# Optimization experiments

Hardware: AMD Instinct MI355X
Metric: run time of the kernel (lower is better)

The kernel has to match this reference:

```python
import jax, jax.numpy as jnp
import numpy as np

B, S, D_MODEL = 2, 2048, 768
N_QK, D_QK = 16, 16
N_OV, D_OV = 256, 1
VKV = 16
ROT_DIM, ROT_BASE = 16, 10000.0
SCALE = D_QK ** 0.5  # attn_scale defaults to sqrt(d_qk_head)


def _rotary_sin_cos(n_ctx, rotary_dim, base):
    # TransformerLens-style, non-adjacent pairs (GPT-NeoX)
    pos = jnp.arange(n_ctx, dtype=jnp.float32)
    dim = jnp.arange(rotary_dim // 2, dtype=jnp.float32)
    freq = base ** (dim / (rotary_dim / 2))
    freq = jnp.concatenate([freq, freq])  # 'd -> (2 d)'
    angles = pos[:, None] / freq[None, :]  # [n_ctx, rotary_dim]
    return jnp.sin(angles), jnp.cos(angles)


def _apply_rotary(x, sin, cos):
    # x: [B, S, H, d_head]; rotate first ROT_DIM dims, pass through the rest
    s = x.shape[1]
    xr = x[..., :ROT_DIM]
    half = ROT_DIM // 2
    rot = jnp.concatenate([-xr[..., half:], xr[..., :half]], axis=-1)  # rotate_every_two (non-adjacent)
    xr = xr * cos[:s, None, :] + rot * sin[:s, None, :]
    return jnp.concatenate([xr, x[..., ROT_DIM:]], axis=-1) if x.shape[-1] > ROT_DIM else xr


def setup_inputs() -> dict:
    key = jax.random.key(0)
    ks = jax.random.split(key, 6)
    std_qk = np.sqrt(2.0 / (D_MODEL * D_QK))   # kaiming fan_in for [H, d_model, d_head]
    std_v = np.sqrt(2.0 / (D_MODEL * D_OV))
    std_o = np.sqrt(2.0 / (D_OV * D_MODEL))
    std_vk = np.sqrt(2.0 / (N_QK * D_QK))
    return {
        "resid": jax.random.normal(ks[0], (B, S, D_MODEL), jnp.float32),
        "W_Q": jax.random.normal(ks[1], (N_QK, D_MODEL, D_QK), jnp.float32) * std_qk,
        "W_K": jax.random.normal(ks[2], (N_QK, D_MODEL, D_QK), jnp.float32) * std_qk,
        "W_V": jax.random.normal(ks[3], (N_OV, D_MODEL, D_OV), jnp.float32) * std_v,
        "W_O": jax.random.normal(ks[4], (N_OV, D_OV, D_MODEL), jnp.float32) * std_o,
        "b_Q": jnp.zeros((N_QK, D_QK), jnp.float32),
        "b_K": jnp.zeros((N_QK, D_QK), jnp.float32),
        "b_V": jnp.zeros((N_OV, D_OV), jnp.float32),
        "b_O": jnp.zeros((D_MODEL,), jnp.float32),
        "virtual_k": jax.random.normal(ks[5], (VKV, N_QK, D_QK), jnp.float32) * std_vk,
        "virtual_v": jnp.zeros((VKV, N_OV, D_OV), jnp.float32),
    }


def reference(resid, W_Q, W_K, W_V, W_O, b_Q, b_K, b_V, b_O, virtual_k, virtual_v):
    b, s, _ = resid.shape
    sin, cos = _rotary_sin_cos(s, ROT_DIM, ROT_BASE)

    q = jnp.einsum('bsd,hde->bshe', resid, W_Q) + b_Q  # [B,S,N_QK,D_QK]
    k = jnp.einsum('bsd,hde->bshe', resid, W_K) + b_K
    v = jnp.einsum('bsd,hde->bshe', resid, W_V) + b_V  # [B,S,N_OV,1]

    q = _apply_rotary(q, sin, cos)
    k = _apply_rotary(k, sin, cos)

    # append virtual KV along key axis
    k = jnp.concatenate([k, jnp.broadcast_to(virtual_k[None], (b, VKV, N_QK, D_QK))], axis=1)
    v = jnp.concatenate([v, jnp.broadcast_to(virtual_v[None], (b, VKV, N_OV, D_OV))], axis=1)

    scores = jnp.einsum('bqhe,bkhe->bhqk', q, k) / SCALE  # [B,H,S,S+VKV]
    i = jnp.arange(s)[:, None]
    j = jnp.arange(s + VKV)[None, :]
    mask = (j - i) <= VKV  # tril(.., diagonal=VKV)
    scores = jnp.where(mask, scores, -jnp.inf)
    pattern = jax.nn.softmax(scores, axis=-1)
    pattern = jnp.where(jnp.isnan(pattern), 0.0, pattern)

    r = N_OV // N_QK
    v_r = v.transpose(0, 2, 1, 3).reshape(b, N_QK, r, s + VKV, D_OV)  # [B,n_qk,r,K,1]
    z = jnp.einsum('bnqk,bnrkh->bnrqh', pattern, v_r)  # [B,n_qk,r,S,1]
    z = z.reshape(b, N_OV, s, D_OV).transpose(0, 2, 1, 3)  # [B,S,N_OV,1]

    out = jnp.einsum('bqhd,hdm->bqm', z, W_O) + b_O  # [B,S,D_MODEL]
    return out
```

## Files before the change

kernel.cpp:

```cpp
#include <hip/hip_runtime.h>
#include <hip/hip_bf16.h>
#include <math.h>

#define B_   2
#define S_   2048
#define DM   768
#define H_   16
#define C_   256
#define VKV_ 16
#define SK   2064
#define SKP  2080
#define NT_  65

#define TSPLIT 16
#define MAXSP  5
#define NACT   164

typedef __attribute__((ext_vector_type(8))) short short8;
typedef __attribute__((ext_vector_type(4))) short short4v;
typedef __attribute__((ext_vector_type(4))) float f32x4;
typedef __attribute__((ext_vector_type(16))) float f32x16;
typedef __attribute__((ext_vector_type(4))) unsigned uint4v;

#define QSCALE 0.360673760222240851f
#define L2B8   1.6609640474436811f

__device__ __forceinline__ short tobf(float f) {
    union { float f; unsigned u; } x; x.f = f;
    unsigned r = x.u + 0x7FFFu + ((x.u >> 16) & 1u);
    return (short)(r >> 16);
}
__device__ __forceinline__ float frombf_lo(unsigned u) {
    union { unsigned u; float f; } x; x.u = u << 16; return x.f;
}
__device__ __forceinline__ float frombf_hi(unsigned u) {
    union { unsigned u; float f; } x; x.u = u & 0xFFFF0000u; return x.f;
}

__device__ __forceinline__ void gload_lds16(const short* g, short* l) {
    __builtin_amdgcn_global_load_lds(
        (const __attribute__((address_space(1))) unsigned int*)g,
        (__attribute__((address_space(3))) unsigned int*)l, 16, 0, 0);
}

#define NRES (4096*768/4)
#define NWQ  (768*768)
#define NWO  (768*256)
__global__ __launch_bounds__(256) void conv_all(
    const float* __restrict__ resid,
    const float* __restrict__ WQ, const float* __restrict__ WK,
    const float* __restrict__ WV, const float* __restrict__ WO,
    const float* __restrict__ bQ, const float* __restrict__ bK,
    const float* __restrict__ bV,
    const float* __restrict__ vKp, const float* __restrict__ vVp,
    short* __restrict__ Ab, short* __restrict__ Wqkv_t,
    short* __restrict__ WtO, float* __restrict__ bqkv,
    short* __restrict__ Kb2, short* __restrict__ Vt3)
{
    int t = blockIdx.x * 256 + threadIdx.x;
    if (t < NRES) {
        float4 v = *(const float4*)(resid + (size_t)t * 4);
        short4v o = { tobf(v.x), tobf(v.y), tobf(v.z), tobf(v.w) };
        *(short4v*)(Ab + (size_t)t * 4) = o;
        return;
    }
    t -= NRES;
    if (t < NWQ) {
        int cc, d;
        if (t < 512 * 768) {
            const int e    = t & 15;
            const int rest = t >> 4;
            d  = rest % 768;
            cc = (rest / 768) * 16 + e;
        } else { cc = t / 768; d = t % 768; }
        float w;
        if (cc < 256)      w = WQ[((size_t)(cc >> 4) * DM + d) * 16 + (cc & 15)];
        else if (cc < 512) w = WK[((size_t)((cc - 256) >> 4) * DM + d) * 16 + (cc & 15)];
        else               w = WV[(size_t)(cc - 512) * DM + d];
        Wqkv_t[(size_t)cc * 768 + d] = tobf(w);
        return;
    }
    t -= NWQ;
    if (t < NWO) {
        int c = t & 255, m = t >> 8;
        WtO[t] = tobf(WO[(size_t)c * DM + m]);
        return;
    }
    t -= NWO;
    if (t < 768) {
        bqkv[t] = (t < 256) ? bQ[t] : (t < 512 ? bK[t - 256] : bV[t - 512]);
        return;
    }
    t -= 768;
    if (t < 32 * 32) {
        const int bh = t >> 5;
        const int s  = S_ + (t & 31);
        const int h  = bh & 15;
        short kb[16], vb[16];
        if (s < SK) {
            const int tt = s - S_;
#pragma unroll
            for (int e = 0; e < 16; ++e) {
                kb[e] = tobf(vKp[(size_t)tt * 256 + h * 16 + e]);
                vb[e] = tobf(vVp[(size_t)tt * 256 + h * 16 + e]);
            }
        } else {
#pragma unroll
            for (int e = 0; e < 16; ++e) { kb[e] = 0; vb[e] = 0; }
        }
        const int t5 = s >> 5;
        short* kbase = Kb2 + ((size_t)bh * NT_ + t5) * 512 + (s & 31) * 8;
#pragma unroll
        for (int e = 0; e < 8; ++e)  { kbase[e] = kb[e]; kbase[256 + e] = kb[e + 8]; }
        short* vbase = Vt3 + ((size_t)bh * NT_ + t5) * 1024
                     + ((s >> 4) & 1) * 512 + ((s >> 3) & 1) * 8 + (s & 7);
#pragma unroll
        for (int dv = 0; dv < 16; ++dv) vbase[dv * 16] = vb[dv];
    }
}

__global__ __launch_bounds__(256) void mm_qkv(
    const short* __restrict__ A, const short* __restrict__ Bt,
    const float* __restrict__ bias,
    short* __restrict__ Qb2, short* __restrict__ Kb2, short* __restrict__ Vt3)
{
    __shared__ float CtS[128][65];
    short* As = (short*)&CtS[0][0];
    short* Bs = (short*)&CtS[0][0] + 8192;

    const int tid  = threadIdx.x;
    const int w    = tid >> 6;
    const int lane = tid & 63;
    const int wm   = w >> 1, wn = w & 1;
    const int g    = lane >> 4, c = lane & 15;

    const int linear = blockIdx.y * 12 + blockIdx.x;
    const int xcd  = linear & 7;
    const int jj2  = linear >> 3;
    const int m0   = (xcd * 4 + jj2 / 12) * 128;
    const int n0   = (jj2 % 12) * 64;

    f32x4 acc[4][2];
#pragma unroll
    for (int i = 0; i < 4; ++i)
#pragma unroll
        for (int j = 0; j < 2; ++j) acc[i][j] = (f32x4){0.f, 0.f, 0.f, 0.f};

    const int lr = lane >> 3;
    const int lc = lane & 7;

    for (int k0 = 0; k0 < 768; k0 += 64) {
#pragma unroll
        for (int i = 0; i < 4; ++i) {
            const int ch  = i * 4 + w;
            const int row = ch * 8 + lr;
            const int scc = lc ^ (row & 7);
            gload_lds16(A + (size_t)(m0 + row) * 768 + k0 + scc * 8, As + ch * 512);
        }
#pragma unroll
        for (int i = 0; i < 2; ++i) {
            const int ch  = i * 4 + w;
            const int row = ch * 8 + lr;
            const int scc = lc ^ (row & 7);
            gload_lds16(Bt + (size_t)(n0 + row) * 768 + k0 + scc * 8, Bs + ch * 512);
        }
        __syncthreads();
#pragma unroll
        for (int kk = 0; kk < 64; kk += 32) {
            short8 af[4], bf[2];
#pragma unroll
            for (int i = 0; i < 4; ++i) {
                const int row = wm * 64 + i * 16 + c;
                const int sc  = ((kk >> 3) + g) ^ (row & 7);
                af[i] = *(const short8*)(As + row * 64 + sc * 8);
            }
#pragma unroll
            for (int j = 0; j < 2; ++j) {
                const int row = wn * 32 + j * 16 + c;
                const int sc  = ((kk >> 3) + g) ^ (row & 7);
                bf[j] = *(const short8*)(Bs + row * 64 + sc * 8);
            }
#pragma unroll
            for (int i = 0; i < 4; ++i)
#pragma unroll
                for (int j = 0; j < 2; ++j)
                    acc[i][j] = __builtin_amdgcn_mfma_f32_16x16x32_bf16(
                        af[i], bf[j], acc[i][j], 0, 0, 0);
        }
        __syncthreads();
    }

#pragma unroll
    for (int i = 0; i < 4; ++i)
#pragma unroll
        for (int j = 0; j < 2; ++j)
#pragma unroll
            for (int r = 0; r < 4; ++r)
                CtS[wm * 64 + i * 16 + 4 * g + r][wn * 32 + j * 16 + c] = acc[i][j][r];
    __syncthreads();

    const int b = m0 >> 11;
    if (n0 < 512) {
        const int isQ   = n0 < 256;
        const int hbase = (n0 & 255) >> 4;
#pragma unroll
        for (int it = 0; it < 2; ++it) {
            const int idx  = it * 256 + tid;
            const int srow = idx & 127;
            const int g16  = idx >> 7;
            const int s    = (m0 + srow) & 2047;
            const int bh   = b * 16 + hbase + g16;
            float v[16];
#pragma unroll
            for (int e = 0; e < 16; ++e)
                v[e] = CtS[srow][g16 * 16 + e] + bias[n0 + g16 * 16 + e];
            union { short s[16]; short8 v8[2]; } u;
#pragma unroll
            for (int e = 0; e < 8; ++e) {
                const float invf = __builtin_amdgcn_exp2f(-(float)e * L2B8);
                float sn, cs;
                __sincosf((float)s * invf, &sn, &cs);
                float o0 = v[e] * cs - v[e + 8] * sn;
                float o1 = v[e + 8] * cs + v[e] * sn;
                if (isQ) { o0 *= QSCALE; o1 *= QSCALE; }
                u.s[e] = tobf(o0); u.s[e + 8] = tobf(o1);
            }
            short* dst = (isQ ? Qb2 + ((size_t)bh * 64 + (s >> 5)) * 512
                              : Kb2 + ((size_t)bh * NT_ + (s >> 5)) * 512)
                       + (s & 31) * 8;
            *(short8*)dst         = u.v8[0];
            *(short8*)(dst + 256) = u.v8[1];
        }
    } else {
        const int hbase = (n0 - 512) >> 4;
#pragma unroll
        for (int it = 0; it < 2; ++it) {
            const int idx = it * 256 + tid;
            const int dvl = idx & 63;
            const int rg  = idx >> 6;
            const int s0  = (m0 + rg * 16) & 2047;
            const int bh  = b * 16 + hbase + (dvl >> 4);
            const float bv = bias[n0 + dvl];
            union { short s[16]; short8 v8[2]; } u;
#pragma unroll
            for (int k = 0; k < 16; ++k)
                u.s[k] = tobf(CtS[rg * 16 + k][dvl] + bv);
            short* dst = Vt3 + ((size_t)bh * NT_ + (s0 >> 5)) * 1024
                       + ((s0 >> 4) & 1) * 512 + (dvl & 15) * 16;
            *(short8*)dst       = u.v8[0];
            *(short8*)(dst + 8) = u.v8[1];
        }
    }
}

__global__ __launch_bounds__(256) void mm_out(
    const short* __restrict__ A, const short* __restrict__ Bt,
    const float* __restrict__ bias, float* __restrict__ Cout)
{
    __shared__ short As[128 * 64];
    __shared__ short Bs[64 * 64];

    const int tid  = threadIdx.x;
    const int w    = tid >> 6;
    const int lane = tid & 63;
    const int wm   = w >> 1, wn = w & 1;
    const int g    = lane >> 4, c = lane & 15;

    const int linear = blockIdx.y * 12 + blockIdx.x;
    const int xcd  = linear & 7;
    const int jj2  = linear >> 3;
    const int m0   = (xcd * 4 + jj2 / 12) * 128;
    const int n0   = (jj2 % 12) * 64;

    f32x4 acc[4][2];
#pragma unroll
    for (int i = 0; i < 4; ++i)
#pragma unroll
        for (int j = 0; j < 2; ++j) acc[i][j] = (f32x4){0.f, 0.f, 0.f, 0.f};

    const int lr = lane >> 3;
    const int lc = lane & 7;

    for (int k0 = 0; k0 < 256; k0 += 64) {
#pragma unroll
        for (int i = 0; i < 4; ++i) {
            const int ch  = i * 4 + w;
            const int row = ch * 8 + lr;
            const int scc = lc ^ (row & 7);
            gload_lds16(A + (size_t)(m0 + row) * 256 + k0 + scc * 8, As + ch * 512);
        }
#pragma unroll
        for (int i = 0; i < 2; ++i) {
            const int ch  = i * 4 + w;
            const int row = ch * 8 + lr;
            const int scc = lc ^ (row & 7);
            gload_lds16(Bt + (size_t)(n0 + row) * 256 + k0 + scc * 8, Bs + ch * 512);
        }
        __syncthreads();
#pragma unroll
        for (int kk = 0; kk < 64; kk += 32) {
            short8 af[4], bf[2];
#pragma unroll
            for (int i = 0; i < 4; ++i) {
                const int row = wm * 64 + i * 16 + c;
                const int sc  = ((kk >> 3) + g) ^ (row & 7);
                af[i] = *(const short8*)(As + row * 64 + sc * 8);
            }
#pragma unroll
            for (int j = 0; j < 2; ++j) {
                const int row = wn * 32 + j * 16 + c;
                const int sc  = ((kk >> 3) + g) ^ (row & 7);
                bf[j] = *(const short8*)(Bs + row * 64 + sc * 8);
            }
#pragma unroll
            for (int i = 0; i < 4; ++i)
#pragma unroll
                for (int j = 0; j < 2; ++j)
                    acc[i][j] = __builtin_amdgcn_mfma_f32_16x16x32_bf16(
                        af[i], bf[j], acc[i][j], 0, 0, 0);
        }
        __syncthreads();
    }
#pragma unroll
    for (int i = 0; i < 4; ++i)
#pragma unroll
        for (int j = 0; j < 2; ++j) {
            const int col = n0 + wn * 32 + j * 16 + c;
            const float bv = bias[col];
#pragma unroll
            for (int r = 0; r < 4; ++r) {
                const int row = m0 + wm * 64 + i * 16 + 4 * g + r;
                Cout[(size_t)row * DM + col] = acc[i][j][r] + bv;
            }
        }
}

__global__ __launch_bounds__(256) void attn_split(
    const short* __restrict__ Qb2, const short* __restrict__ Kb2,
    const short* __restrict__ Vt3, unsigned* __restrict__ PartA,
    float* __restrict__ PartL)
{
    const int w    = threadIdx.x >> 6;
    const int lane = threadIdx.x & 63;
    const int blk  = blockIdx.x;
    const int xcd  = blk & 7;
    const int j    = blk >> 3;
    const int bhl  = j / 41;
    const int slot = j - bhl * 41;
    const int bh   = xcd * 4 + bhl;
    const int r    = slot * 4 + w;
    int qt, sp;
    if (r < 49)       { sp = 1; qt = 15 + r; }
    else if (r < 82)  { sp = 2; qt = 31 + (r - 49); }
    else if (r < 99)  { sp = 3; qt = 47 + (r - 82); }
    else if (r == 99) { sp = 4; qt = 63; }
    else              { sp = 0; qt = 163 - r; }

    const int nt   = qt + 2;
    const int t0   = sp * TSPLIT;
    const int tend = min(t0 + TSPLIT, nt);

    const int hi = lane >> 5;
    const int qc = lane & 31;
    const int q0 = qt * 32;

    const f32x16 zero16 = {0,0,0,0,0,0,0,0,0,0,0,0,0,0,0,0};

    short8 qf = *(const short8*)(Qb2 + ((size_t)bh * 64 + qt) * 512 + lane * 8);

    f32x16 acc = zero16;
    float lsum = 0.f;

    const short* kbase = Kb2 + (size_t)bh * NT_ * 512 + lane * 8;
    const short* vbase = Vt3 + (size_t)bh * NT_ * 1024 + (lane & 15) * 16 + hi * 8;
    const int qv16  = q0 + qc + 16;
    const int tmask = (q0 + 17) >> 5;

#define LK(tt)  (*(const short8*)(kbase + (size_t)(tt) * 512))
#define LVA(tt) (*(const short8*)(vbase + (size_t)(tt) * 1024))
#define LVB(tt) (*(const short8*)(vbase + (size_t)(tt) * 1024 + 512))

#define SOFTMAX_TILE(S, tt, B1, B2)                                          \
    {                                                                        \
        if ((tt) >= tmask) {                                                 \
            const int kt_ = (tt) * 32;                                       \
            _Pragma("unroll")                                                \
            for (int rr = 0; rr < 16; ++rr) {                                \
                const int key = kt_ + (rr & 3) + 8 * (rr >> 2) + 4 * hi;     \
                S[rr] = (key <= qv16) ? S[rr] : -INFINITY;                   \
            }                                                                \
        }                                                                    \
        unsigned pk[8];                                                      \
        _Pragma("unroll")                                                    \
        for (int jj = 0; jj < 8; ++jj) {                                     \
            const float p0 = __builtin_amdgcn_exp2f(S[2 * jj]);              \
            const float p1 = __builtin_amdgcn_exp2f(S[2 * jj + 1]);          \
            lsum += p0 + p1;                                                 \
            asm("v_cvt_pk_bf16_f32 %0, %1, %2" : "=v"(pk[jj]) : "v"(p0), "v"(p1)); \
        }                                                                    \
        unsigned a0 = pk[0], a2 = pk[2], a1 = pk[1], a3 = pk[3];             \
        unsigned a4 = pk[4], a6 = pk[6], a5 = pk[5], a7 = pk[7];             \
        asm("v_permlane32_swap_b32 %0, %1" : "+v"(a0), "+v"(a2));            \
        asm("v_permlane32_swap_b32 %0, %1" : "+v"(a1), "+v"(a3));            \
        asm("v_permlane32_swap_b32 %0, %1" : "+v"(a4), "+v"(a6));            \
        asm("v_permlane32_swap_b32 %0, %1" : "+v"(a5), "+v"(a7));            \
        B1.u[0] = a0; B1.u[1] = a1; B1.u[2] = a2; B1.u[3] = a3;              \
        B2.u[0] = a4; B2.u[1] = a5; B2.u[2] = a6; B2.u[3] = a7;              \
    }

    const int npair_end = t0 + ((tend - t0) & ~1);

    if (t0 < npair_end) {
        short8 kfA = LK(t0),     vaA = LVA(t0),     vvA = LVB(t0);
        short8 kfB = LK(t0 + 1), vaB = LVA(t0 + 1), vvB = LVB(t0 + 1);

        for (int t = t0; t < npair_end; t += 2) {
            short8 kfA_n = kfA, vaA_n = vaA, vvA_n = vvA;
            short8 kfB_n = kfB, vaB_n = vaB, vvB_n = vvB;
            if (t + 2 < npair_end) {
                kfA_n = LK(t + 2); vaA_n = LVA(t + 2); vvA_n = LVB(t + 2);
                kfB_n = LK(t + 3); vaB_n = LVA(t + 3); vvB_n = LVB(t + 3);
            }

            __builtin_amdgcn_s_setprio(1);
            f32x16 S0 = __builtin_amdgcn_mfma_f32_32x32x16_bf16(kfA, qf, zero16, 0, 0, 0);
            f32x16 S1 = __builtin_amdgcn_mfma_f32_32x32x16_bf16(kfB, qf, zero16, 0, 0, 0);
            __builtin_amdgcn_s_setprio(0);

            union { unsigned u[4]; short8 v; } b1A, b2A, b1B, b2B;
            SOFTMAX_TILE(S0, t,     b1A, b2A);
            SOFTMAX_TILE(S1, t + 1, b1B, b2B);

            __builtin_amdgcn_s_setprio(1);
            acc = __builtin_amdgcn_mfma_f32_32x32x16_bf16(vaA, b1A.v, acc, 0, 0, 0);
            acc = __builtin_amdgcn_mfma_f32_32x32x16_bf16(vvA, b2A.v, acc, 0, 0, 0);
            acc = __builtin_amdgcn_mfma_f32_32x32x16_bf16(vaB, b1B.v, acc, 0, 0, 0);
            acc = __builtin_amdgcn_mfma_f32_32x32x16_bf16(vvB, b2B.v, acc, 0, 0, 0);
            __builtin_amdgcn_s_setprio(0);

            kfA = kfA_n; vaA = vaA_n; vvA = vvA_n;
            kfB = kfB_n; vaB = vaB_n; vvB = vvB_n;
        }
    }
    if (npair_end < tend) {
        const int t = npair_end;
        short8 kf = LK(t), va = LVA(t), vv = LVB(t);
        f32x16 S0 = __builtin_amdgcn_mfma_f32_32x32x16_bf16(kf, qf, zero16, 0, 0, 0);
        union { unsigned u[4]; short8 v; } b1, b2;
        SOFTMAX_TILE(S0, t, b1, b2);
        acc = __builtin_amdgcn_mfma_f32_32x32x16_bf16(va, b1.v, acc, 0, 0, 0);
        acc = __builtin_amdgcn_mfma_f32_32x32x16_bf16(vv, b2.v, acc, 0, 0, 0);
    }

    uint4v pa;
    asm("v_cvt_pk_bf16_f32 %0, %1, %2" : "=v"(pa.x) : "v"(acc[0]), "v"(acc[1]));
    asm("v_cvt_pk_bf16_f32 %0, %1, %2" : "=v"(pa.y) : "v"(acc[2]), "v"(acc[3]));
    asm("v_cvt_pk_bf16_f32 %0, %1, %2" : "=v"(pa.z) : "v"(acc[4]), "v"(acc[5]));
    asm("v_cvt_pk_bf16_f32 %0, %1, %2" : "=v"(pa.w) : "v"(acc[6]), "v"(acc[7]));

    const int pidx = (bh * 64 + qt) * MAXSP + sp;
    *(uint4v*)(PartA + ((size_t)pidx * 64 + lane) * 4) = pa;

    lsum += __shfl_xor(lsum, 32);
    if (hi == 0) PartL[(size_t)pidx * 32 + qc] = lsum;
}

__global__ __launch_bounds__(256) void attn_combine(
    const unsigned* __restrict__ PartA, const float* __restrict__ PartL,
    short* __restrict__ Zb)
{
    const int w    = threadIdx.x >> 6;
    const int lane = threadIdx.x & 63;
    const int wid  = blockIdx.x * 4 + w;
    const int bh   = wid >> 6;
    const int qt   = wid & 63;
    const int hi   = lane >> 5;
    const int qc   = lane & 31;
    const int ns   = (qt + 2 + TSPLIT - 1) / TSPLIT;

    float a[8];
#pragma unroll
    for (int rr = 0; rr < 8; ++rr) a[rr] = 0.f;
    float lsum = 0.f;

    const int pbase = (bh * 64 + qt) * MAXSP;
    for (int sp = 0; sp < ns; ++sp) {
        uint4v pa = *(const uint4v*)(PartA + ((size_t)(pbase + sp) * 64 + lane) * 4);
        a[0] += frombf_lo(pa.x); a[1] += frombf_hi(pa.x);
        a[2] += frombf_lo(pa.y); a[3] += frombf_hi(pa.y);
        a[4] += frombf_lo(pa.z); a[5] += frombf_hi(pa.z);
        a[6] += frombf_lo(pa.w); a[7] += frombf_hi(pa.w);
        lsum += PartL[(size_t)(pbase + sp) * 32 + qc];
    }
    const float inv = 1.f / lsum;

    const int b = bh >> 4, h = bh & 15;
    const int q0 = qt * 32;
    short* zp = Zb + ((size_t)(b * S_ + q0 + qc)) * C_ + h * 16;
    unsigned o01, o23, o45, o67;
    {
        float a0 = a[0] * inv, a1 = a[1] * inv, a2 = a[2] * inv, a3 = a[3] * inv;
        float a4 = a[4] * inv, a5 = a[5] * inv, a6 = a[6] * inv, a7 = a[7] * inv;
        asm("v_cvt_pk_bf16_f32 %0, %1, %2" : "=v"(o01) : "v"(a0), "v"(a1));
        asm("v_cvt_pk_bf16_f32 %0, %1, %2" : "=v"(o23) : "v"(a2), "v"(a3));
        asm("v_cvt_pk_bf16_f32 %0, %1, %2" : "=v"(o45) : "v"(a4), "v"(a5));
        asm("v_cvt_pk_bf16_f32 %0, %1, %2" : "=v"(o67) : "v"(a6), "v"(a7));
    }
    *(unsigned*)(zp + 4 * hi)         = o01;
    *(unsigned*)(zp + 4 * hi + 2)     = o23;
    *(unsigned*)(zp + 8 + 4 * hi)     = o45;
    *(unsigned*)(zp + 8 + 4 * hi + 2) = o67;
}

extern "C" void kernel_launch(void* const* d_in, const int* in_sizes, int n_in,
                              void* d_out, int out_size, void* d_ws, size_t ws_size,
                              hipStream_t stream)
{
    const float* resid = (const float*)d_in[0];
    const float* WQ = (const float*)d_in[1];
    const float* WK = (const float*)d_in[2];
    const float* WV = (const float*)d_in[3];
    const float* WO = (const float*)d_in[4];
    const float* bQ = (const float*)d_in[5];
    const float* bK = (const float*)d_in[6];
    const float* bV = (const float*)d_in[7];
    const float* bO = (const float*)d_in[8];
    const float* vK = (const float*)d_in[9];
    const float* vV = (const float*)d_in[10];
    float* out = (float*)d_out;
    float* ws  = (float*)d_ws;

    short* Zb   = (short*)ws;
    float* bqkv = ws + 3145728;
    short* Ab   = (short*)(ws + 3145728 + 768);
    short* Wqt  = Ab + 3145728;
    short* WtO  = Wqt + 589824;
    short* Qb2  = WtO + 196608;
    short* Kb2  = Qb2 + 1048576;
    short* Vt3  = Kb2 + 1064960;
    unsigned* PartA = (unsigned*)(Vt3 + 2129920);
    float*    PartL = (float*)(PartA + 2621440);

    const int conv_total = NRES + NWQ + NWO + 768 + 1024;
    conv_all<<<dim3((conv_total + 255) / 256), 256, 0, stream>>>(
        resid, WQ, WK, WV, WO, bQ, bK, bV, vK, vV,
        Ab, Wqt, WtO, bqkv, Kb2, Vt3);
    mm_qkv<<<dim3(12, 32), 256, 0, stream>>>(Ab, Wqt, bqkv, Qb2, Kb2, Vt3);
    attn_split<<<dim3(32 * NACT / 4), 256, 0, stream>>>(Qb2, Kb2, Vt3, PartA, PartL);
    attn_combine<<<dim3(512), 256, 0, stream>>>(PartA, PartL, Zb);
    mm_out<<<dim3(12, 32), 256, 0, stream>>>(Zb, WtO, bO, out);
}
```

Baseline: 58.21 us.

## Halve GEMM M-tiles and finalize single-split attention tiles in-place

Both the QKV and output GEMMs now use 64-row M tiles instead of 128, doubling the grid from 384 to 768 blocks so the 256 CUs are better filled. The attention split kernel now normalizes and writes Z directly for query tiles that have only one split (qt<=14). The combine kernel is launched only over the 49 multi-split tiles per head, which removes partial-buffer traffic and combine work for those early tiles. Smaller GEMM tiles reduce data reuse per block and add more per-block overhead.

```diff
diff --git a/kernel.cpp b/kernel.cpp
--- a/kernel.cpp
+++ b/kernel.cpp
@@ -124,9 +124,9 @@
     const float* __restrict__ bias,
     short* __restrict__ Qb2, short* __restrict__ Kb2, short* __restrict__ Vt3)
 {
-    __shared__ float CtS[128][65];
+    __shared__ float CtS[64][65];
     short* As = (short*)&CtS[0][0];
-    short* Bs = (short*)&CtS[0][0] + 8192;
+    short* Bs = As + 4096;
 
     const int tid  = threadIdx.x;
     const int w    = tid >> 6;
@@ -137,12 +137,12 @@
     const int linear = blockIdx.y * 12 + blockIdx.x;
     const int xcd  = linear & 7;
     const int jj2  = linear >> 3;
-    const int m0   = (xcd * 4 + jj2 / 12) * 128;
+    const int m0   = (xcd * 8 + jj2 / 12) * 64;
     const int n0   = (jj2 % 12) * 64;
 
-    f32x4 acc[4][2];
-#pragma unroll
-    for (int i = 0; i < 4; ++i)
+    f32x4 acc[2][2];
+#pragma unroll
+    for (int i = 0; i < 2; ++i)
 #pragma unroll
         for (int j = 0; j < 2; ++j) acc[i][j] = (f32x4){0.f, 0.f, 0.f, 0.f};
 
@@ -151,7 +151,7 @@
 
     for (int k0 = 0; k0 < 768; k0 += 64) {
 #pragma unroll
-        for (int i = 0; i < 4; ++i) {
+        for (int i = 0; i < 2; ++i) {
             const int ch  = i * 4 + w;
             const int row = ch * 8 + lr;
             const int scc = lc ^ (row & 7);
@@ -167,10 +167,10 @@
         __syncthreads();
 #pragma unroll
         for (int kk = 0; kk < 64; kk += 32) {
-            short8 af[4], bf[2];
-#pragma unroll
-            for (int i = 0; i < 4; ++i) {
-                const int row = wm * 64 + i * 16 + c;
+            short8 af[2], bf[2];
+#pragma unroll
+            for (int i = 0; i < 2; ++i) {
+                const int row = wm * 32 + i * 16 + c;
                 const int sc  = ((kk >> 3) + g) ^ (row & 7);
                 af[i] = *(const short8*)(As + row * 64 + sc * 8);
             }
@@ -181,7 +181,7 @@
                 bf[j] = *(const short8*)(Bs + row * 64 + sc * 8);
             }
 #pragma unroll
-            for (int i = 0; i < 4; ++i)
+            for (int i = 0; i < 2; ++i)
 #pragma unroll
                 for (int j = 0; j < 2; ++j)
                     acc[i][j] = __builtin_amdgcn_mfma_f32_16x16x32_bf16(
@@ -191,65 +191,57 @@
     }
 
 #pragma unroll
-    for (int i = 0; i < 4; ++i)
+    for (int i = 0; i < 2; ++i)
 #pragma unroll
         for (int j = 0; j < 2; ++j)
 #pragma unroll
             for (int r = 0; r < 4; ++r)
-                CtS[wm * 64 + i * 16 + 4 * g + r][wn * 32 + j * 16 + c] = acc[i][j][r];
+                CtS[wm * 32 + i * 16 + 4 * g + r][wn * 32 + j * 16 + c] = acc[i][j][r];
     __syncthreads();
 
     const int b = m0 >> 11;
     if (n0 < 512) {
         const int isQ   = n0 < 256;
         const int hbase = (n0 & 255) >> 4;
-#pragma unroll
-        for (int it = 0; it < 2; ++it) {
-            const int idx  = it * 256 + tid;
-            const int srow = idx & 127;
-            const int g16  = idx >> 7;
-            const int s    = (m0 + srow) & 2047;
-            const int bh   = b * 16 + hbase + g16;
-            float v[16];
-#pragma unroll
-            for (int e = 0; e < 16; ++e)
-                v[e] = CtS[srow][g16 * 16 + e] + bias[n0 + g16 * 16 + e];
-            union { short s[16]; short8 v8[2]; } u;
-#pragma unroll
-            for (int e = 0; e < 8; ++e) {
-                const float invf = __builtin_amdgcn_exp2f(-(float)e * L2B8);
-                float sn, cs;
-                __sincosf((float)s * invf, &sn, &cs);
-                float o0 = v[e] * cs - v[e + 8] * sn;
-                float o1 = v[e + 8] * cs + v[e] * sn;
-                if (isQ) { o0 *= QSCALE; o1 *= QSCALE; }
-                u.s[e] = tobf(o0); u.s[e + 8] = tobf(o1);
-            }
-            short* dst = (isQ ? Qb2 + ((size_t)bh * 64 + (s >> 5)) * 512
-                              : Kb2 + ((size_t)bh * NT_ + (s >> 5)) * 512)
-                       + (s & 31) * 8;
-            *(short8*)dst         = u.v8[0];
-            *(short8*)(dst + 256) = u.v8[1];
-        }
+        const int srow = tid & 63;
+        const int g16  = tid >> 6;
+        const int s    = (m0 + srow) & 2047;
+        const int bh   = b * 16 + hbase + g16;
+        float v[16];
+#pragma unroll
+        for (int e = 0; e < 16; ++e)
+            v[e] = CtS[srow][g16 * 16 + e] + bias[n0 + g16 * 16 + e];
+        union { short s[16]; short8 v8[2]; } u;
+#pragma unroll
+        for (int e = 0; e < 8; ++e) {
+            const float invf = __builtin_amdgcn_exp2f(-(float)e * L2B8);
+            float sn, cs;
+            __sincosf((float)s * invf, &sn, &cs);
+            float o0 = v[e] * cs - v[e + 8] * sn;
+            float o1 = v[e + 8] * cs + v[e] * sn;
+            if (isQ) { o0 *= QSCALE; o1 *= QSCALE; }
+            u.s[e] = tobf(o0); u.s[e + 8] = tobf(o1);
+        }
+        short* dst = (isQ ? Qb2 + ((size_t)bh * 64 + (s >> 5)) * 512
+                          : Kb2 + ((size_t)bh * NT_ + (s >> 5)) * 512)
+                   + (s & 31) * 8;
+        *(short8*)dst         = u.v8[0];
+        *(short8*)(dst + 256) = u.v8[1];
     } else {
         const int hbase = (n0 - 512) >> 4;
-#pragma unroll
-        for (int it = 0; it < 2; ++it) {
-            const int idx = it * 256 + tid;
-            const int dvl = idx & 63;
-            const int rg  = idx >> 6;
-            const int s0  = (m0 + rg * 16) & 2047;
-            const int bh  = b * 16 + hbase + (dvl >> 4);
-            const float bv = bias[n0 + dvl];
-            union { short s[16]; short8 v8[2]; } u;
-#pragma unroll
-            for (int k = 0; k < 16; ++k)
-                u.s[k] = tobf(CtS[rg * 16 + k][dvl] + bv);
-            short* dst = Vt3 + ((size_t)bh * NT_ + (s0 >> 5)) * 1024
-                       + ((s0 >> 4) & 1) * 512 + (dvl & 15) * 16;
-            *(short8*)dst       = u.v8[0];
-            *(short8*)(dst + 8) = u.v8[1];
-        }
+        const int dvl = tid & 63;
+        const int rg  = tid >> 6;
+        const int s0  = (m0 + rg * 16) & 2047;
+        const int bh  = b * 16 + hbase + (dvl >> 4);
+        const float bv = bias[n0 + dvl];
+        union { short s[16]; short8 v8[2]; } u;
+#pragma unroll
+        for (int k = 0; k < 16; ++k)
+            u.s[k] = tobf(CtS[rg * 16 + k][dvl] + bv);
+        short* dst = Vt3 + ((size_t)bh * NT_ + (s0 >> 5)) * 1024
+                   + ((s0 >> 4) & 1) * 512 + (dvl & 15) * 16;
+        *(short8*)dst       = u.v8[0];
+        *(short8*)(dst + 8) = u.v8[1];
     }
 }
 
@@ -257,8 +249,8 @@
     const short* __restrict__ A, const short* __restrict__ Bt,
     const float* __restrict__ bias, float* __restrict__ Cout)
 {
-    __shared__ short As[128 * 64];
-    __shared__ short Bs[64 * 64];
+    __shared__ short As[4096];
+    __shared__ short Bs[4096];
 
     const int tid  = threadIdx.x;
     const int w    = tid >> 6;
@@ -269,12 +261,12 @@
     const int linear = blockIdx.y * 12 + blockIdx.x;
     const int xcd  = linear & 7;
     const int jj2  = linear >> 3;
-    const int m0   = (xcd * 4 + jj2 / 12) * 128;
+    const int m0   = (xcd * 8 + jj2 / 12) * 64;
     const int n0   = (jj2 % 12) * 64;
 
-    f32x4 acc[4][2];
-#pragma unroll
-    for (int i = 0; i < 4; ++i)
+    f32x4 acc[2][2];
+#pragma unroll
+    for (int i = 0; i < 2; ++i)
 #pragma unroll
         for (int j = 0; j < 2; ++j) acc[i][j] = (f32x4){0.f, 0.f, 0.f, 0.f};
 
@@ -283,7 +275,7 @@
 
     for (int k0 = 0; k0 < 256; k0 += 64) {
 #pragma unroll
-        for (int i = 0; i < 4; ++i) {
+        for (int i = 0; i < 2; ++i) {
             const int ch  = i * 4 + w;
             const int row = ch * 8 + lr;
             const int scc = lc ^ (row & 7);
@@ -299,10 +291,10 @@
         __syncthreads();
 #pragma unroll
         for (int kk = 0; kk < 64; kk += 32) {
-            short8 af[4], bf[2];
-#pragma unroll
-            for (int i = 0; i < 4; ++i) {
-                const int row = wm * 64 + i * 16 + c;
+            short8 af[2], bf[2];
+#pragma unroll
+            for (int i = 0; i < 2; ++i) {
+                const int row = wm * 32 + i * 16 + c;
                 const int sc  = ((kk >> 3) + g) ^ (row & 7);
                 af[i] = *(const short8*)(As + row * 64 + sc * 8);
             }
@@ -313,7 +305,7 @@
                 bf[j] = *(const short8*)(Bs + row * 64 + sc * 8);
             }
 #pragma unroll
-            for (int i = 0; i < 4; ++i)
+            for (int i = 0; i < 2; ++i)
 #pragma unroll
                 for (int j = 0; j < 2; ++j)
                     acc[i][j] = __builtin_amdgcn_mfma_f32_16x16x32_bf16(
@@ -322,14 +314,14 @@
         __syncthreads();
     }
 #pragma unroll
-    for (int i = 0; i < 4; ++i)
+    for (int i = 0; i < 2; ++i)
 #pragma unroll
         for (int j = 0; j < 2; ++j) {
             const int col = n0 + wn * 32 + j * 16 + c;
             const float bv = bias[col];
 #pragma unroll
             for (int r = 0; r < 4; ++r) {
-                const int row = m0 + wm * 64 + i * 16 + 4 * g + r;
+                const int row = m0 + wm * 32 + i * 16 + 4 * g + r;
                 Cout[(size_t)row * DM + col] = acc[i][j][r] + bv;
             }
         }
@@ -338,7 +330,7 @@
 __global__ __launch_bounds__(256) void attn_split(
     const short* __restrict__ Qb2, const short* __restrict__ Kb2,
     const short* __restrict__ Vt3, unsigned* __restrict__ PartA,
-    float* __restrict__ PartL)
+    float* __restrict__ PartL, short* __restrict__ Zb)
 {
     const int w    = threadIdx.x >> 6;
     const int lane = threadIdx.x & 63;
@@ -452,6 +444,26 @@
         acc = __builtin_amdgcn_mfma_f32_32x32x16_bf16(vv, b2.v, acc, 0, 0, 0);
     }
 
+    lsum += __shfl_xor(lsum, 32);
+
+    if (sp == 0 && qt <= 14) {
+        const float inv = 1.f / lsum;
+        const int b = bh >> 4, h = bh & 15;
+        short* zp = Zb + ((size_t)(b * S_ + q0 + qc)) * C_ + h * 16;
+        unsigned o01, o23, o45, o67;
+        float a0 = acc[0] * inv, a1 = acc[1] * inv, a2 = acc[2] * inv, a3 = acc[3] * inv;
+        float a4 = acc[4] * inv, a5 = acc[5] * inv, a6 = acc[6] * inv, a7 = acc[7] * inv;
+        asm("v_cvt_pk_bf16_f32 %0, %1, %2" : "=v"(o01) : "v"(a0), "v"(a1));
+        asm("v_cvt_pk_bf16_f32 %0, %1, %2" : "=v"(o23) : "v"(a2), "v"(a3));
+        asm("v_cvt_pk_bf16_f32 %0, %1, %2" : "=v"(o45) : "v"(a4), "v"(a5));
+        asm("v_cvt_pk_bf16_f32 %0, %1, %2" : "=v"(o67) : "v"(a6), "v"(a7));
+        *(unsigned*)(zp + 4 * hi)         = o01;
+        *(unsigned*)(zp + 4 * hi + 2)     = o23;
+        *(unsigned*)(zp + 8 + 4 * hi)     = o45;
+        *(unsigned*)(zp + 8 + 4 * hi + 2) = o67;
+        return;
+    }
+
     uint4v pa;
     asm("v_cvt_pk_bf16_f32 %0, %1, %2" : "=v"(pa.x) : "v"(acc[0]), "v"(acc[1]));
     asm("v_cvt_pk_bf16_f32 %0, %1, %2" : "=v"(pa.y) : "v"(acc[2]), "v"(acc[3]));
@@ -460,8 +472,6 @@
 
     const int pidx = (bh * 64 + qt) * MAXSP + sp;
     *(uint4v*)(PartA + ((size_t)pidx * 64 + lane) * 4) = pa;
-
-    lsum += __shfl_xor(lsum, 32);
     if (hi == 0) PartL[(size_t)pidx * 32 + qc] = lsum;
 }
 
@@ -472,8 +482,8 @@
     const int w    = threadIdx.x >> 6;
     const int lane = threadIdx.x & 63;
     const int wid  = blockIdx.x * 4 + w;
-    const int bh   = wid >> 6;
-    const int qt   = wid & 63;
+    const int bh   = wid / 49;
+    const int qt   = 15 + (wid - bh * 49);
     const int hi   = lane >> 5;
     const int qc   = lane & 31;
     const int ns   = (qt + 2 + TSPLIT - 1) / TSPLIT;
@@ -545,8 +555,8 @@
     conv_all<<<dim3((conv_total + 255) / 256), 256, 0, stream>>>(
         resid, WQ, WK, WV, WO, bQ, bK, bV, vK, vV,
         Ab, Wqt, WtO, bqkv, Kb2, Vt3);
-    mm_qkv<<<dim3(12, 32), 256, 0, stream>>>(Ab, Wqt, bqkv, Qb2, Kb2, Vt3);
-    attn_split<<<dim3(32 * NACT / 4), 256, 0, stream>>>(Qb2, Kb2, Vt3, PartA, PartL);
-    attn_combine<<<dim3(512), 256, 0, stream>>>(PartA, PartL, Zb);
-    mm_out<<<dim3(12, 32), 256, 0, stream>>>(Zb, WtO, bO, out);
-}
+    mm_qkv<<<dim3(12, 64), 256, 0, stream>>>(Ab, Wqt, bqkv, Qb2, Kb2, Vt3);
+    attn_split<<<dim3(32 * NACT / 4), 256, 0, stream>>>(Qb2, Kb2, Vt3, PartA, PartL, Zb);
+    attn_combine<<<dim3(392), 256, 0, stream>>>(PartA, PartL, Zb);
+    mm_out<<<dim3(12, 64), 256, 0, stream>>>(Zb, WtO, bO, out);
+}
```

Result: faster. 55.47 us (median of 3 runs) (-4.7%).
